# Performance work log

Hardware: AMD Instinct MI355X
Metric: run time of the kernel (lower is better)

## Reference

```python
import jax, jax.numpy as jnp
import numpy as np

B_SZ, C, H, W = 64, 256, 28, 28
HEADS, HEAD_DIM = 4, 64
BLOCK, HALO = 4, 4
WIN = BLOCK + 2 * HALO  # 12
KCONV = 3


def _unfold(x, k, s, p):
    # torch F.unfold semantics; returns [b, c, oh, kh, ow, kw]
    b, c, h, w = x.shape
    xp = jnp.pad(x, ((0, 0), (0, 0), (p, p), (p, p)))
    oh = (h + 2 * p - k) // s + 1
    ow = (w + 2 * p - k) // s + 1
    ih = jnp.arange(oh)[:, None] * s + jnp.arange(k)[None, :]
    iw = jnp.arange(ow)[:, None] * s + jnp.arange(k)[None, :]
    pt = xp[:, :, ih]            # [b,c,oh,kh,Wp]
    pt = pt[:, :, :, :, iw]      # [b,c,oh,kh,ow,kw]
    return pt


def _rel_to_abs(x):
    # x: [b, l, 2r-1] -> [b, l, r] via shift trick
    b, l, m = x.shape
    r = (m + 1) // 2
    x = jnp.pad(x, ((0, 0), (0, 0), (0, 1))).reshape(b, l * (m + 1))
    x = jnp.pad(x, ((0, 0), (0, m - l))).reshape(b, l + 1, m)
    return x[:, :l, -r:]


def _relative_logits_1d(q, rel_k):
    # q: [b, x, y, d], rel_k: [2r-1, d] -> [b, x, i(=r), y, j(=r)]
    b, h, w, _ = q.shape
    r = (rel_k.shape[0] + 1) // 2
    logits = jnp.einsum('bxyd,rd->bxyr', q, rel_k)
    logits = _rel_to_abs(logits.reshape(b * h, w, 2 * r - 1)).reshape(b, h, w, r)
    return jnp.broadcast_to(logits[:, :, None], (b, h, r, w, r))


def _rel_pos_emb(q, rel_height, rel_width):
    # q: [B, block^2, d]
    B, n, d = q.shape
    qb = q.reshape(B, BLOCK, BLOCK, d)
    lw = _relative_logits_1d(qb, rel_width)                 # [B,x,i,y,j]
    lw = lw.transpose(0, 1, 3, 2, 4).reshape(B, n, -1)      # b (x y) (i j)
    qh = qb.transpose(0, 2, 1, 3)
    lh = _relative_logits_1d(qh, rel_height)                # [B,y,i,x,j]
    lh = lh.transpose(0, 3, 1, 4, 2).reshape(B, n, -1)      # b (y x) (j i)
    return lw + lh


def setup_inputs() -> dict:
    key = jax.random.key(0)
    ks = jax.random.split(key, 13)
    f = jnp.float32
    rel_scale = HEAD_DIM ** (-0.5)
    return {
        'x': jax.random.normal(ks[0], (B_SZ, C, H, W), dtype=f),
        'w1': jax.random.normal(ks[1], (C, C), dtype=f) * 0.05,
        'b1': jax.random.normal(ks[2], (C,), dtype=f) * 0.05,
        'w2': jax.random.normal(ks[3], (C, C), dtype=f) * 0.05,
        'b2': jax.random.normal(ks[4], (C,), dtype=f) * 0.05,
        'w3': jax.random.normal(ks[5], (C, C), dtype=f) * 0.05,
        'b3': jax.random.normal(ks[6], (C,), dtype=f) * 0.05,
        'fc_w': jax.random.normal(ks[7], (KCONV * KCONV, 3 * HEADS), dtype=f) * 0.1,
        'dep_w': jax.random.normal(ks[8], (C, KCONV * KCONV, KCONV, KCONV), dtype=f) * 0.05,
        'rel_height': jax.random.normal(ks[9], (2 * WIN - 1, HEAD_DIM), dtype=f) * rel_scale,
        'rel_width': jax.random.normal(ks[10], (2 * WIN - 1, HEAD_DIM), dtype=f) * rel_scale,
        'rate1': jax.random.normal(ks[11], (1,), dtype=f),
        'rate2': jax.random.normal(ks[12], (1,), dtype=f),
    }


def reference(x, w1, b1, w2, b2, w3, b3, fc_w, dep_w, rel_height, rel_width, rate1, rate2):
    b = x.shape[0]
    scaling = HEAD_DIM ** (-0.5)
    q = jnp.einsum('bchw,oc->bohw', x, w1) + b1[None, :, None, None]
    k = jnp.einsum('bchw,oc->bohw', x, w2) + b2[None, :, None, None]
    v = jnp.einsum('bchw,oc->bohw', x, w3) + b3[None, :, None, None]
    c = q.shape[1]
    nb = H // BLOCK          # 7 blocks per side
    nwin = nb * nb           # 49 windows
    n_q = BLOCK * BLOCK      # 16 queries per window
    n_k = WIN * WIN          # 144 keys per window (with halo)

    # block queries: b c (h p1) (w p2) -> (b h w) (p1 p2) c
    q_att = q.reshape(b, c, nb, BLOCK, nb, BLOCK).transpose(0, 2, 4, 3, 5, 1).reshape(b * nwin, n_q, c)
    kp = _unfold(k, WIN, BLOCK, HALO).transpose(0, 2, 4, 3, 5, 1).reshape(b * nwin, n_k, c)
    vp = _unfold(v, WIN, BLOCK, HALO).transpose(0, 2, 4, 3, 5, 1).reshape(b * nwin, n_k, c)

    def split_heads(t):
        Bn, n, _ = t.shape
        return t.reshape(Bn, n, HEADS, HEAD_DIM).transpose(0, 2, 1, 3).reshape(Bn * HEADS, n, HEAD_DIM)

    q1 = split_heads(q_att) * scaling
    k1 = split_heads(kp)
    v1 = split_heads(vp)

    sim = jnp.einsum('bid,bjd->bij', q1, k1)
    sim = sim + _rel_pos_emb(q1, rel_height, rel_width)

    # NOTE: faithfully reproduces original (valid positions get -max, padded get 0)
    ones = jnp.ones((1, 1, H, W), x.dtype)
    valid = _unfold(ones, WIN, BLOCK, HALO).transpose(0, 2, 4, 3, 5, 1).reshape(nwin, n_k) > 0
    big_neg = -jnp.finfo(sim.dtype).max
    sim = sim.reshape(b, nwin, HEADS, n_q, n_k)
    sim = jnp.where(valid[None, :, None, None, :], big_neg, sim)
    attn = jax.nn.softmax(sim, axis=-1).reshape(b * nwin * HEADS, n_q, n_k)

    out = jnp.einsum('bij,bjd->bid', attn, v1)
    out = out.reshape(b * nwin, HEADS, n_q, HEAD_DIM).transpose(0, 2, 1, 3)  # merge heads
    out = out.reshape(b, nb, nb, BLOCK, BLOCK, c)
    out_att = out.transpose(0, 5, 1, 3, 2, 4).reshape(b, c, H, W)

    # conv branch: fc over concatenated per-head q,k,v, then depthwise-grouped conv
    f_all = jnp.concatenate([
        q.reshape(b, HEADS, HEAD_DIM, H * W),
        k.reshape(b, HEADS, HEAD_DIM, H * W),
        v.reshape(b, HEADS, HEAD_DIM, H * W)], axis=1)        # [b, 3*heads, hd, HW]
    f_all = jnp.einsum('bcmn,oc->bomn', f_all, fc_w)          # [b, 9, hd, HW]
    f_conv = f_all.transpose(0, 2, 1, 3).reshape(b, HEAD_DIM * KCONV * KCONV, H, W)
    out_conv = jax.lax.conv_general_dilated(
        f_conv, dep_w, window_strides=(1, 1), padding=((1, 1), (1, 1)),
        dimension_numbers=('NCHW', 'OIHW', 'NCHW'), feature_group_count=HEAD_DIM)

    return rate1[0] * out_att + rate2[0] * out_conv
```

## Files before the change

kernel.cpp:

```cpp
#include <hip/hip_runtime.h>
#include <hip/hip_bf16.h>

typedef __hip_bfloat16 bf16;
typedef unsigned int uint;
typedef unsigned short ushort;

using frag8 = __attribute__((ext_vector_type(8))) short;
using f32x4 = __attribute__((ext_vector_type(4))) float;

#define HWH 784

__global__ __launch_bounds__(256) void fold_w2(const float* __restrict__ fc_w,
                                               const float* __restrict__ dep_w,
                                               const float* __restrict__ b1,
                                               const float* __restrict__ b2,
                                               const float* __restrict__ b3,
                                               float* __restrict__ W2,
                                               float* __restrict__ biascat) {
    int idx = blockIdx.x * 256 + threadIdx.x;
    if (idx < 768) {
        const float* bs = idx < 256 ? b1 : (idx < 512 ? b2 : b3);
        biascat[idx] = bs[idx & 255];
    }
    if (idx >= 256 * 108) return;
    int oc  = idx / 108;
    int r   = idx % 108;
    int c12 = r / 9;
    int k9  = r % 9;
    float s = 0.f;
#pragma unroll
    for (int o = 0; o < 9; ++o)
        s += fc_w[o * 12 + c12] * dep_w[oc * 81 + o * 9 + k9];
    W2[idx] = s;
}

__global__ __launch_bounds__(256) void wprep(const float* __restrict__ w1,
                                             const float* __restrict__ w2,
                                             const float* __restrict__ w3,
                                             bf16* __restrict__ wbf) {
    int row = blockIdx.x, tid = threadIdx.x;
    const float* src = row < 256 ? w1 : (row < 512 ? w2 : w3);
    wbf[row * 256 + tid] = __float2bfloat16(src[(row & 255) * 256 + tid]);
}

__global__ __launch_bounds__(256) void xpose(const float* __restrict__ x,
                                             bf16* __restrict__ xT) {
    __shared__ float t[32][33];
    const int n0 = blockIdx.x * 32, c0 = blockIdx.y * 32, b = blockIdx.z;
    const int tid = threadIdx.x;
    const float* xb = x + (size_t)b * (256 * HWH);
#pragma unroll
    for (int e = tid; e < 1024; e += 256) {
        int r = e >> 5, col = e & 31;
        int n = n0 + col;
        t[r][col] = (n < HWH) ? xb[(size_t)(c0 + r) * HWH + n] : 0.f;
    }
    __syncthreads();
#pragma unroll
    for (int e = tid; e < 512; e += 256) {
        int r = e >> 4, cp = (e & 15) * 2;
        int n = n0 + r;
        if (n < HWH) {
            __hip_bfloat162 h;
            h.x = __float2bfloat16(t[cp][r]);
            h.y = __float2bfloat16(t[cp + 1][r]);
            *reinterpret_cast<__hip_bfloat162*>(
                &xT[((size_t)b * HWH + n) * 256 + c0 + cp]) = h;
        }
    }
}

__device__ inline void load_lds16(const bf16* g, short* lds) {
    __builtin_amdgcn_global_load_lds(
        (const __attribute__((address_space(1))) void*)g,
        (__attribute__((address_space(3))) void*)lds, 16, 0, 0);
}

__global__ __launch_bounds__(256) void gemm_mfma(const bf16* __restrict__ wbf,
                                                 const float* __restrict__ biascat,
                                                 const bf16* __restrict__ xT,
                                                 bf16* __restrict__ perm) {
    __shared__ short lds[8192];

    const int tid  = threadIdx.x;
    const int wave = tid >> 6, lane = tid & 63;
    const int b    = blockIdx.z;
    const int m0   = blockIdx.y * 128;
    const int n0   = blockIdx.x * 128;
    const int mw   = wave & 1, nw = wave >> 1;
    const int lrow = lane & 15, lkc = lane >> 4;

    f32x4 acc[4][4] = {};
    const bf16* xb = xT + (size_t)b * (HWH * 256);

    for (int k0 = 0; k0 < 256; k0 += 32) {
#pragma unroll
        for (int i = 0; i < 2; ++i) {
            const int jb = 2 * wave + i;
            const bf16* ga = wbf + (size_t)(m0 + 16 * jb + lrow) * 256 + k0 + lkc * 8;
            load_lds16(ga, &lds[jb * 512]);
            int n = n0 + 16 * jb + lrow;
            if (n > HWH - 1) n = HWH - 1;
            const bf16* gb = xb + (size_t)n * 256 + k0 + lkc * 8;
            load_lds16(gb, &lds[4096 + jb * 512]);
        }
        __syncthreads();

        frag8 af[4], bf_[4];
#pragma unroll
        for (int i = 0; i < 4; ++i)
            af[i] = *reinterpret_cast<const frag8*>(&lds[(4 * mw + i) * 512 + lane * 8]);
#pragma unroll
        for (int j = 0; j < 4; ++j)
            bf_[j] = *reinterpret_cast<const frag8*>(&lds[4096 + (4 * nw + j) * 512 + lane * 8]);
#pragma unroll
        for (int i = 0; i < 4; ++i)
#pragma unroll
            for (int j = 0; j < 4; ++j)
                acc[i][j] = __builtin_amdgcn_mfma_f32_16x16x32_bf16(
                    af[i], bf_[j], acc[i][j], 0, 0, 0);
        __syncthreads();
    }

#pragma unroll
    for (int i = 0; i < 4; ++i) {
        const int rowb = m0 + mw * 64 + i * 16 + lkc * 4;
        bf16* dsts[4]; float bias4[4];
#pragma unroll
        for (int r = 0; r < 4; ++r) {
            const int m = rowb + r;
            const int sec = m >> 8, ch = m & 255;
            dsts[r] = perm + (((size_t)b * 64 + (ch & 63)) * 12 + sec * 4 + (ch >> 6)) * HWH;
            bias4[r] = biascat[m];
        }
#pragma unroll
        for (int j = 0; j < 4; ++j) {
            const int col = n0 + nw * 64 + j * 16 + lrow;
            if (col < HWH) {
#pragma unroll
                for (int r = 0; r < 4; ++r)
                    dsts[r][col] = __float2bfloat16(acc[i][j][r] + bias4[r]);
            }
        }
    }
}

__global__ __launch_bounds__(256) void out_fused4(
    const bf16* __restrict__ perm, const float* __restrict__ W2,
    const float* __restrict__ rate1, const float* __restrict__ rate2,
    float* __restrict__ out) {
    __shared__ __align__(16) short plane[12][1020];
    __shared__ float w2s2[4][12][12];
    __shared__ float attb[4][49];
    __shared__ __align__(16) short vatt[4][784];

    const int g = blockIdx.x, b = blockIdx.y, tid = threadIdx.x;
    const ushort zero_bf = 0;

    for (int e = tid; e < 576; e += 256) {
        int oc = e / 144, rem = e % 144, c = rem / 12, k = rem % 12;
        w2s2[oc][c][k] = (k < 9) ? W2[(4 * g + oc) * 108 + c * 9 + k] : 0.f;
    }
    if (tid < 196) attb[tid / 49][tid % 49] = 0.f;
    for (int e = tid; e < 1392; e += 256) {
        int c12 = e / 116, u = e % 116, idx;
        if (u < 30)      idx = u;
        else if (u < 60) idx = 29 * 34 + (u - 30);
        else { int v = u - 60; idx = ((v >> 1) + 1) * 34 + (v & 1) * 29; }
        plane[c12][idx] = (short)zero_bf;
    }
    {
        const uint4* src = (const uint4*)(perm + ((size_t)b * 64 + g) * 12 * HWH);
        for (int e = tid; e < 1176; e += 256) {
            int c12 = e / 98, u = e % 98;
            uint4 q = src[e];
            ushort s8[8] = {(ushort)(q.x & 0xffff), (ushort)(q.x >> 16),
                            (ushort)(q.y & 0xffff), (ushort)(q.y >> 16),
                            (ushort)(q.z & 0xffff), (ushort)(q.z >> 16),
                            (ushort)(q.w & 0xffff), (ushort)(q.w >> 16)};
            int p = u * 8, y = p / 28, x = p - y * 28;
            int ry = y + 1, cx = x + 1;
            short* pl = &plane[c12][0];
#pragma unroll
            for (int t4 = 0; t4 < 8; ++t4) {
                pl[ry * 34 + cx] = (short)s8[t4];
                if (++cx == 29) { cx = 1; ++ry; }
            }
        }
    }
    for (int e = tid; e < 392; e += 256) {
        int oc = e / 98, u = e % 98;
        int c = 4 * g + oc;
        const uint4* src = (const uint4*)(
            perm + (((size_t)b * 64 + (c & 63)) * 12 + 8 + (c >> 6)) * HWH);
        reinterpret_cast<uint4*>(&vatt[oc][0])[u] = src[u];
    }
    __syncthreads();

    if (tid < 100) {
        int oc = tid / 25, w = tid % 25;
        int wi = w / 5 + 1, wj = w % 5 + 1;
        int r0 = 4 * wi - 4, c0 = 4 * wj - 4;
        float s = 0.f;
#pragma unroll
        for (int r = 0; r < 12; ++r) {
            const __hip_bfloat162* pv =
                (const __hip_bfloat162*)&vatt[oc][(r0 + r) * 28 + c0];
#pragma unroll
            for (int q = 0; q < 6; ++q) {
                float2 f = __bfloat1622float2(pv[q]);
                s += f.x + f.y;
            }
        }
        attb[oc][wi * 7 + wj] = s * (1.0f / 144.0f);
    }

    float acc[4][4] = {};
    const int y = tid % 28, xs = tid / 28, x0 = xs * 4;
    if (tid < 196) {
#pragma unroll
        for (int c = 0; c < 12; ++c) {
            float rr[3][6];
#pragma unroll
            for (int dy = 0; dy < 3; ++dy) {
                const uint* row = (const uint*)&plane[c][(y + dy) * 34 + x0];
#pragma unroll
                for (int jp = 0; jp < 3; ++jp) {
                    uint w = row[jp];
                    float2 f = __bfloat1622float2(*(const __hip_bfloat162*)&w);
                    rr[dy][2 * jp]     = f.x;
                    rr[dy][2 * jp + 1] = f.y;
                }
            }
#pragma unroll
            for (int oc = 0; oc < 4; ++oc) {
                const float4* wr = reinterpret_cast<const float4*>(&w2s2[oc][c][0]);
                float4 wa = wr[0], wb = wr[1], wc = wr[2];
                const float wk[9] = {wa.x, wa.y, wa.z, wa.w, wb.x, wb.y, wb.z, wb.w, wc.x};
#pragma unroll
                for (int ky = 0; ky < 3; ++ky)
#pragma unroll
                    for (int kx = 0; kx < 3; ++kx) {
                        float wv = wk[ky * 3 + kx];
#pragma unroll
                        for (int px = 0; px < 4; ++px)
                            acc[oc][px] += wv * rr[ky][px + kx];
                    }
            }
        }
    }
    __syncthreads();

    if (tid < 196) {
        const float r1 = rate1[0], r2 = rate2[0];
        const int wi = y >> 2, wj = xs;
#pragma unroll
        for (int oc = 0; oc < 4; ++oc) {
            float av = attb[oc][wi * 7 + wj] * r1;
            float4 o;
            o.x = av + r2 * acc[oc][0];
            o.y = av + r2 * acc[oc][1];
            o.z = av + r2 * acc[oc][2];
            o.w = av + r2 * acc[oc][3];
            *reinterpret_cast<float4*>(
                &out[((size_t)(b * 256 + 4 * g + oc)) * HWH + y * 28 + x0]) = o;
        }
    }
}

extern "C" void kernel_launch(void* const* d_in, const int* in_sizes, int n_in,
                              void* d_out, int out_size, void* d_ws, size_t ws_size,
                              hipStream_t stream) {
    const float* x     = (const float*)d_in[0];
    const float* w1    = (const float*)d_in[1];
    const float* b1    = (const float*)d_in[2];
    const float* w2    = (const float*)d_in[3];
    const float* b2    = (const float*)d_in[4];
    const float* w3    = (const float*)d_in[5];
    const float* b3    = (const float*)d_in[6];
    const float* fc_w  = (const float*)d_in[7];
    const float* dep_w = (const float*)d_in[8];
    const float* rate1 = (const float*)d_in[11];
    const float* rate2 = (const float*)d_in[12];
    float* out = (float*)d_out;

    char* wsb = (char*)d_ws;
    bf16*  perm    = (bf16*)wsb;
    bf16*  xT      = (bf16*)(wsb + 77070336);
    bf16*  wbf     = (bf16*)(wsb + 102760448);
    float* W2      = (float*)(wsb + 103153664);
    float* biascat = (float*)(wsb + 103264256);

    fold_w2  <<<dim3(108),        dim3(256), 0, stream>>>(fc_w, dep_w, b1, b2, b3, W2, biascat);
    wprep    <<<dim3(768),        dim3(256), 0, stream>>>(w1, w2, w3, wbf);
    xpose    <<<dim3(25, 8, 64),  dim3(256), 0, stream>>>(x, xT);
    gemm_mfma<<<dim3(7, 6, 64),   dim3(256), 0, stream>>>(wbf, biascat, xT, perm);
    out_fused4<<<dim3(64, 64),    dim3(256), 0, stream>>>(perm, W2, rate1, rate2, out);
}
```

Measured before the change: 255.9 us.

## Enlarge GEMM tile to 256x128 with linear grid and pack conv FMAs

The MFMA GEMM moves from 128x128 tiles to 256x128 tiles. Each wave now owns 64 rows across all 128 columns, with 32 accumulators per wave and a flattened 1D grid ordered so that tiles sharing the same M block are adjacent. The goal is more reuse of the B tile loaded into LDS and fewer blocks, at the cost of higher register pressure and possibly lower occupancy. Separately, the depthwise 3x3 conv accumulation in the output kernel is rewritten with float2 vectors so the compiler can emit packed FMA instructions.

```diff
diff --git a/kernel.cpp b/kernel.cpp
--- a/kernel.cpp
+++ b/kernel.cpp
@@ -7,6 +7,7 @@
 
 using frag8 = __attribute__((ext_vector_type(8))) short;
 using f32x4 = __attribute__((ext_vector_type(4))) float;
+using f32x2 = __attribute__((ext_vector_type(2))) float;
 
 #define HWH 784
 
@@ -76,47 +77,54 @@
         (__attribute__((address_space(3))) void*)lds, 16, 0, 0);
 }
 
-__global__ __launch_bounds__(256) void gemm_mfma(const bf16* __restrict__ wbf,
-                                                 const float* __restrict__ biascat,
-                                                 const bf16* __restrict__ xT,
-                                                 bf16* __restrict__ perm) {
-    __shared__ short lds[8192];
+__global__ __launch_bounds__(256) void gemm_mfma2(const bf16* __restrict__ wbf,
+                                                  const float* __restrict__ biascat,
+                                                  const bf16* __restrict__ xT,
+                                                  bf16* __restrict__ perm) {
+    __shared__ short lds[12288];
 
     const int tid  = threadIdx.x;
     const int wave = tid >> 6, lane = tid & 63;
-    const int b    = blockIdx.z;
-    const int m0   = blockIdx.y * 128;
-    const int n0   = blockIdx.x * 128;
-    const int mw   = wave & 1, nw = wave >> 1;
+    const int lin  = blockIdx.x;
+    const int mt   = lin / 448;
+    const int rem  = lin - mt * 448;
+    const int b    = rem / 7;
+    const int nt   = rem - b * 7;
+    const int m0   = mt * 256;
+    const int n0   = nt * 128;
     const int lrow = lane & 15, lkc = lane >> 4;
 
-    f32x4 acc[4][4] = {};
+    f32x4 acc[4][8] = {};
     const bf16* xb = xT + (size_t)b * (HWH * 256);
 
     for (int k0 = 0; k0 < 256; k0 += 32) {
+#pragma unroll
+        for (int i = 0; i < 4; ++i) {
+            const int jb = 4 * wave + i;
+            const bf16* ga = wbf + (size_t)(m0 + 16 * jb + lrow) * 256 + k0 + lkc * 8;
+            load_lds16(ga, &lds[jb * 512]);
+        }
 #pragma unroll
         for (int i = 0; i < 2; ++i) {
             const int jb = 2 * wave + i;
-            const bf16* ga = wbf + (size_t)(m0 + 16 * jb + lrow) * 256 + k0 + lkc * 8;
-            load_lds16(ga, &lds[jb * 512]);
             int n = n0 + 16 * jb + lrow;
             if (n > HWH - 1) n = HWH - 1;
             const bf16* gb = xb + (size_t)n * 256 + k0 + lkc * 8;
-            load_lds16(gb, &lds[4096 + jb * 512]);
+            load_lds16(gb, &lds[8192 + jb * 512]);
         }
         __syncthreads();
 
-        frag8 af[4], bf_[4];
+        frag8 af[4], bf_[8];
 #pragma unroll
         for (int i = 0; i < 4; ++i)
-            af[i] = *reinterpret_cast<const frag8*>(&lds[(4 * mw + i) * 512 + lane * 8]);
-#pragma unroll
-        for (int j = 0; j < 4; ++j)
-            bf_[j] = *reinterpret_cast<const frag8*>(&lds[4096 + (4 * nw + j) * 512 + lane * 8]);
+            af[i] = *reinterpret_cast<const frag8*>(&lds[(4 * wave + i) * 512 + lane * 8]);
+#pragma unroll
+        for (int j = 0; j < 8; ++j)
+            bf_[j] = *reinterpret_cast<const frag8*>(&lds[8192 + j * 512 + lane * 8]);
 #pragma unroll
         for (int i = 0; i < 4; ++i)
 #pragma unroll
-            for (int j = 0; j < 4; ++j)
+            for (int j = 0; j < 8; ++j)
                 acc[i][j] = __builtin_amdgcn_mfma_f32_16x16x32_bf16(
                     af[i], bf_[j], acc[i][j], 0, 0, 0);
         __syncthreads();
@@ -124,7 +132,7 @@
 
 #pragma unroll
     for (int i = 0; i < 4; ++i) {
-        const int rowb = m0 + mw * 64 + i * 16 + lkc * 4;
+        const int rowb = m0 + wave * 64 + i * 16 + lkc * 4;
         bf16* dsts[4]; float bias4[4];
 #pragma unroll
         for (int r = 0; r < 4; ++r) {
@@ -134,8 +142,8 @@
             bias4[r] = biascat[m];
         }
 #pragma unroll
-        for (int j = 0; j < 4; ++j) {
-            const int col = n0 + nw * 64 + j * 16 + lrow;
+        for (int j = 0; j < 8; ++j) {
+            const int col = n0 + j * 16 + lrow;
             if (col < HWH) {
 #pragma unroll
                 for (int r = 0; r < 4; ++r)
@@ -145,7 +153,7 @@
     }
 }
 
-__global__ __launch_bounds__(256) void out_fused4(
+__global__ __launch_bounds__(256) void out_fused5(
     const bf16* __restrict__ perm, const float* __restrict__ W2,
     const float* __restrict__ rate1, const float* __restrict__ rate2,
     float* __restrict__ out) {
@@ -155,7 +163,6 @@
     __shared__ __align__(16) short vatt[4][784];
 
     const int g = blockIdx.x, b = blockIdx.y, tid = threadIdx.x;
-    const ushort zero_bf = 0;
 
     for (int e = tid; e < 576; e += 256) {
         int oc = e / 144, rem = e % 144, c = rem / 12, k = rem % 12;
@@ -167,7 +174,7 @@
         if (u < 30)      idx = u;
         else if (u < 60) idx = 29 * 34 + (u - 30);
         else { int v = u - 60; idx = ((v >> 1) + 1) * 34 + (v & 1) * 29; }
-        plane[c12][idx] = (short)zero_bf;
+        plane[c12][idx] = 0;
     }
     {
         const uint4* src = (const uint4*)(perm + ((size_t)b * 64 + g) * 12 * HWH);
@@ -215,12 +222,12 @@
         attb[oc][wi * 7 + wj] = s * (1.0f / 144.0f);
     }
 
-    float acc[4][4] = {};
+    f32x2 acc2[4][2] = {};
     const int y = tid % 28, xs = tid / 28, x0 = xs * 4;
     if (tid < 196) {
 #pragma unroll
         for (int c = 0; c < 12; ++c) {
-            float rr[3][6];
+            f32x2 rr2[3][3], sh[3][2];
 #pragma unroll
             for (int dy = 0; dy < 3; ++dy) {
                 const uint* row = (const uint*)&plane[c][(y + dy) * 34 + x0];
@@ -228,9 +235,10 @@
                 for (int jp = 0; jp < 3; ++jp) {
                     uint w = row[jp];
                     float2 f = __bfloat1622float2(*(const __hip_bfloat162*)&w);
-                    rr[dy][2 * jp]     = f.x;
-                    rr[dy][2 * jp + 1] = f.y;
+                    rr2[dy][jp] = f32x2{f.x, f.y};
                 }
+                sh[dy][0] = f32x2{rr2[dy][0].y, rr2[dy][1].x};
+                sh[dy][1] = f32x2{rr2[dy][1].y, rr2[dy][2].x};
             }
 #pragma unroll
             for (int oc = 0; oc < 4; ++oc) {
@@ -238,14 +246,17 @@
                 float4 wa = wr[0], wb = wr[1], wc = wr[2];
                 const float wk[9] = {wa.x, wa.y, wa.z, wa.w, wb.x, wb.y, wb.z, wb.w, wc.x};
 #pragma unroll
-                for (int ky = 0; ky < 3; ++ky)
-#pragma unroll
-                    for (int kx = 0; kx < 3; ++kx) {
-                        float wv = wk[ky * 3 + kx];
-#pragma unroll
-                        for (int px = 0; px < 4; ++px)
-                            acc[oc][px] += wv * rr[ky][px + kx];
-                    }
+                for (int ky = 0; ky < 3; ++ky) {
+                    f32x2 w0 = {wk[ky * 3 + 0], wk[ky * 3 + 0]};
+                    f32x2 w1 = {wk[ky * 3 + 1], wk[ky * 3 + 1]};
+                    f32x2 w2v = {wk[ky * 3 + 2], wk[ky * 3 + 2]};
+                    acc2[oc][0] += w0 * rr2[ky][0];
+                    acc2[oc][1] += w0 * rr2[ky][1];
+                    acc2[oc][0] += w1 * sh[ky][0];
+                    acc2[oc][1] += w1 * sh[ky][1];
+                    acc2[oc][0] += w2v * rr2[ky][1];
+                    acc2[oc][1] += w2v * rr2[ky][2];
+                }
             }
         }
     }
@@ -258,10 +269,10 @@
         for (int oc = 0; oc < 4; ++oc) {
             float av = attb[oc][wi * 7 + wj] * r1;
             float4 o;
-            o.x = av + r2 * acc[oc][0];
-            o.y = av + r2 * acc[oc][1];
-            o.z = av + r2 * acc[oc][2];
-            o.w = av + r2 * acc[oc][3];
+            o.x = av + r2 * acc2[oc][0].x;
+            o.y = av + r2 * acc2[oc][0].y;
+            o.z = av + r2 * acc2[oc][1].x;
+            o.w = av + r2 * acc2[oc][1].y;
             *reinterpret_cast<float4*>(
                 &out[((size_t)(b * 256 + 4 * g + oc)) * HWH + y * 28 + x0]) = o;
         }
@@ -291,9 +302,9 @@
     float* W2      = (float*)(wsb + 103153664);
     float* biascat = (float*)(wsb + 103264256);
 
-    fold_w2  <<<dim3(108),        dim3(256), 0, stream>>>(fc_w, dep_w, b1, b2, b3, W2, biascat);
-    wprep    <<<dim3(768),        dim3(256), 0, stream>>>(w1, w2, w3, wbf);
-    xpose    <<<dim3(25, 8, 64),  dim3(256), 0, stream>>>(x, xT);
-    gemm_mfma<<<dim3(7, 6, 64),   dim3(256), 0, stream>>>(wbf, biascat, xT, perm);
-    out_fused4<<<dim3(64, 64),    dim3(256), 0, stream>>>(perm, W2, rate1, rate2, out);
-}
+    fold_w2   <<<dim3(108),        dim3(256), 0, stream>>>(fc_w, dep_w, b1, b2, b3, W2, biascat);
+    wprep     <<<dim3(768),        dim3(256), 0, stream>>>(w1, w2, w3, wbf);
+    xpose     <<<dim3(25, 8, 64),  dim3(256), 0, stream>>>(x, xT);
+    gemm_mfma2<<<dim3(1344),       dim3(256), 0, stream>>>(wbf, biascat, xT, perm);
+    out_fused5<<<dim3(64, 64),     dim3(256), 0, stream>>>(perm, W2, rate1, rate2, out);
+}
```

Result: slower. 279.9 us (+9.4%).
